# Kernel tuning notes

Measured on AMD Instinct MI355X. Metric: run time of the kernel, lower is better.

Reference implementation:

```python
import jax, jax.numpy as jnp
import numpy as np

KS = 4          # kernel_size per pseudo-dim (open linear B-splines, degree 1)
GRID = 28       # level-0 grid side
BATCH = 256     # number of graphs
NUM_FIRST_FC = 49


def _grid(n, B):
    """Batched 8-neighborhood grid graph with 2D pseudo-coords in [0,1]."""
    rs, cs = np.meshgrid(np.arange(n), np.arange(n), indexing='ij')
    idx = rs * n + cs
    src_l, dst_l, ps_l = [], [], []
    for dr in (-1, 0, 1):
        for dc in (-1, 0, 1):
            if dr == 0 and dc == 0:
                continue
            r2, c2 = rs + dr, cs + dc
            ok = (r2 >= 0) & (r2 < n) & (c2 >= 0) & (c2 < n)
            src_l.append(idx[ok])
            dst_l.append((r2 * n + c2)[ok])
            m = int(ok.sum())
            ps_l.append(np.stack([np.full(m, (dr + 1) / 2.0),
                                  np.full(m, (dc + 1) / 2.0)], 1))
    src = np.concatenate(src_l)
    dst = np.concatenate(dst_l)
    pseudo = np.concatenate(ps_l).astype(np.float32)
    off = (np.arange(B) * n * n)[:, None]
    src_b = (src[None] + off).reshape(-1)
    dst_b = (dst[None] + off).reshape(-1)
    return (np.stack([src_b, dst_b]).astype(np.int32),
            np.tile(pseudo, (B, 1)))


def _cluster(n, B):
    """Factor-4 (2x2 block) graclus-style cluster assignment, batched."""
    rs, cs = np.meshgrid(np.arange(n), np.arange(n), indexing='ij')
    c = ((rs // 2) * (n // 2) + (cs // 2)).reshape(-1)
    off = (np.arange(B) * (n // 2) ** 2)[:, None]
    return (c[None] + off).reshape(-1).astype(np.int32)


def setup_inputs() -> dict:
    key = jax.random.key(0)
    ks = jax.random.split(key, 16)
    e0, p0 = _grid(GRID, BATCH)          # 28x28 level
    e1, p1 = _grid(GRID // 2, BATCH)     # 14x14 level
    c0 = _cluster(GRID, BATCH)           # 784 -> 196 per graph
    c1 = _cluster(GRID // 2, BATCH)      # 196 -> 49 per graph
    N0 = BATCH * GRID * GRID
    s = 0.1
    inp = {
        'x': jax.random.normal(ks[0], (N0, 1), jnp.float32),
        'edge_index0': jnp.asarray(e0), 'pseudo0': jnp.asarray(p0),
        'edge_index1': jnp.asarray(e1), 'pseudo1': jnp.asarray(p1),
        'cluster0': jnp.asarray(c0), 'cluster1': jnp.asarray(c1),
        'W1': s * jax.random.normal(ks[1], (16, 1, 32), jnp.float32),
        'root1': s * jax.random.normal(ks[2], (1, 32), jnp.float32),
        'b1': jnp.zeros((32,), jnp.float32),
        'W2': s * jax.random.normal(ks[3], (16, 32, 32), jnp.float32),
        'root2': s * jax.random.normal(ks[4], (32, 32), jnp.float32),
        'b2': jnp.zeros((32,), jnp.float32),
        'W3': s * jax.random.normal(ks[5], (16, 32, 64), jnp.float32),
        'root3': s * jax.random.normal(ks[6], (32, 64), jnp.float32),
        'b3': jnp.zeros((64,), jnp.float32),
        'W4': s * jax.random.normal(ks[7], (16, 64, 64), jnp.float32),
        'root4': s * jax.random.normal(ks[8], (64, 64), jnp.float32),
        'b4': jnp.zeros((64,), jnp.float32),
        'fc1_W': s * jax.random.normal(ks[9], (NUM_FIRST_FC * 64, 512), jnp.float32),
        'fc1_b': jnp.zeros((512,), jnp.float32),
        'fc2_W': s * jax.random.normal(ks[10], (512, 10), jnp.float32),
        'fc2_b': jnp.zeros((10,), jnp.float32),
    }
    return inp


def spline_conv(x, src, dst, pseudo, W, root, bias):
    """SplineGCN layer: degree-1 open B-spline weighting over 2D pseudo-coords,
    mean aggregation over incoming edges, plus root weight and bias."""
    n = x.shape[0]
    pos = pseudo * (KS - 1)                       # [E,2] in [0, KS-1]
    i0f = jnp.clip(jnp.floor(pos), 0, KS - 2)
    frac = pos - i0f                              # [E,2]
    i0 = i0f.astype(jnp.int32)
    XW = jnp.einsum('ni,kio->kno', x, W)          # [K, N, out]: per-kernel transform
    msg = jnp.zeros((src.shape[0], W.shape[2]), x.dtype)
    for a in (0, 1):
        wa = frac[:, 0] if a else 1.0 - frac[:, 0]
        for b in (0, 1):
            wb = frac[:, 1] if b else 1.0 - frac[:, 1]
            k = (i0[:, 0] + a) * KS + (i0[:, 1] + b)     # flat kernel index [E]
            msg = msg + (wa * wb)[:, None] * XW[k, src]  # gather per-edge
    agg = jax.ops.segment_sum(msg, dst, num_segments=n)
    deg = jax.ops.segment_sum(jnp.ones_like(dst, dtype=x.dtype), dst,
                              num_segments=n)
    return agg / jnp.maximum(deg, 1.0)[:, None] + x @ root + bias


def pool4(x, cluster):
    # GraclusMaxPool(2): two halving levels == factor-4 cluster max-pool
    return jax.ops.segment_max(x, cluster, num_segments=x.shape[0] // 4)


def reference(x, edge_index0, pseudo0, edge_index1, pseudo1, cluster0, cluster1,
              W1, root1, b1, W2, root2, b2, W3, root3, b3, W4, root4, b4,
              fc1_W, fc1_b, fc2_W, fc2_b):
    s0, d0 = edge_index0[0], edge_index0[1]
    s1, d1 = edge_index1[0], edge_index1[1]
    h = jax.nn.elu(spline_conv(x, s0, d0, pseudo0, W1, root1, b1))
    h = jax.nn.elu(spline_conv(h, s0, d0, pseudo0, W2, root2, b2))
    h = pool4(h, cluster0)
    h = jax.nn.elu(spline_conv(h, s1, d1, pseudo1, W3, root3, b3))
    h = jax.nn.elu(spline_conv(h, s1, d1, pseudo1, W4, root4, b4))
    h = pool4(h, cluster1)
    h = h.reshape(-1, NUM_FIRST_FC * 64)           # [B, 49*64]
    h = jax.nn.elu(h @ fc1_W + fc1_b)
    # dropout is identity in eval / deterministic reference
    logits = h @ fc2_W + fc2_b
    return jax.nn.log_softmax(logits, axis=-1)
```

## Files before the change

kernel.cpp:

```cpp
#include <hip/hip_runtime.h>

typedef unsigned short u16;
typedef short bf16x8 __attribute__((ext_vector_type(8)));
typedef float f32x4 __attribute__((ext_vector_type(4)));

__device__ __constant__ const int DRS[8] = {-1,-1,-1, 0, 0, 1, 1, 1};
__device__ __constant__ const int DCS[8] = {-1, 0, 1,-1, 1,-1, 0, 1};

__device__ inline float bf2f(u16 u) { return __uint_as_float(((unsigned)u) << 16); }
__device__ inline u16 f2bf(float f) {
  unsigned u = __float_as_uint(f);
  return (u16)((u + 0x7fffu + ((u >> 16) & 1u)) >> 16);
}
__device__ inline float eluf(float v) { return v > 0.f ? v : (__expf(v) - 1.f); }
__device__ inline unsigned pk2(float a, float b) {
  return (unsigned)f2bf(a) | ((unsigned)f2bf(b) << 16);
}

__device__ inline float weff_val(const float* __restrict__ W, int d, int off, int stride) {
  int dd = d >= 4 ? d + 1 : d;
  int dr = dd / 3 - 1, dc = dd - (dd / 3) * 3 - 1;
  int kr0, kr1, nr; float wr0, wr1;
  if (dr < 0)       { kr0 = 0; wr0 = 1.f; kr1 = 0; wr1 = 0.f; nr = 1; }
  else if (dr == 0) { kr0 = 1; wr0 = .5f; kr1 = 2; wr1 = .5f; nr = 2; }
  else              { kr0 = 3; wr0 = 1.f; kr1 = 0; wr1 = 0.f; nr = 1; }
  int kc0, kc1, nc; float wc0, wc1;
  if (dc < 0)       { kc0 = 0; wc0 = 1.f; kc1 = 0; wc1 = 0.f; nc = 1; }
  else if (dc == 0) { kc0 = 1; wc0 = .5f; kc1 = 2; wc1 = .5f; nc = 2; }
  else              { kc0 = 3; wc0 = 1.f; kc1 = 0; wc1 = 0.f; nc = 1; }
  float acc = wr0 * wc0 * W[(kr0 * 4 + kc0) * stride + off];
  if (nc == 2) acc += wr0 * wc1 * W[(kr0 * 4 + kc1) * stride + off];
  if (nr == 2) {
    acc += wr1 * wc0 * W[(kr1 * 4 + kc0) * stride + off];
    if (nc == 2) acc += wr1 * wc1 * W[(kr1 * 4 + kc1) * stride + off];
  }
  return acc;
}

__device__ inline int kperm32(int p) { return (p >> 1) + ((p & 1) << 4); }

__global__ __launch_bounds__(256) void pack_all(
    const float* __restrict__ W1,
    const float* __restrict__ W2, const float* __restrict__ rt2,
    const float* __restrict__ W3, const float* __restrict__ rt3,
    const float* __restrict__ W4, const float* __restrict__ rt4,
    const float* __restrict__ fcW,
    float* __restrict__ wf1, u16* __restrict__ wp2,
    u16* __restrict__ wp3, u16* __restrict__ wp4, u16* __restrict__ wfc) {
  __shared__ u16 T[32 * 514];
  int blk = blockIdx.x, t = threadIdx.x;
  if (blk < 98) {
    int q = blk;
#pragma unroll
    for (int i = 0; i < 16; ++i) {
      int idx = i * 1024 + t * 4;
      int k = idx >> 9, n = idx & 511;
      float4 v = *reinterpret_cast<const float4*>(fcW + (size_t)(q * 32 + k) * 512 + n);
      T[k * 514 + n]     = f2bf(v.x);
      T[k * 514 + n + 1] = f2bf(v.y);
      T[k * 514 + n + 2] = f2bf(v.z);
      T[k * 514 + n + 3] = f2bf(v.w);
    }
    __syncthreads();
#pragma unroll
    for (int w = 0; w < 8; ++w) {
      int g = w * 256 + t;
      int nt = g >> 6, l = g & 63;
      union { int4 q4; u16 s[8]; } R;
#pragma unroll
      for (int j = 0; j < 8; ++j)
        R.s[j] = T[((l >> 4) * 8 + j) * 514 + nt * 16 + (l & 15)];
      *reinterpret_cast<int4*>(wfc + ((size_t)(q * 32 + nt) * 64 + l) * 8) = R.q4;
    }
    return;
  }
  int idx = (blk - 98) * 256 + t;
  if (idx < 256) {
    int d = idx >> 5, o = idx & 31;
    wf1[idx] = weff_val(W1, d, o, 32);
    return;
  }
  if (idx < 9472) {
    int local = idx - 256;
    int j = local & 7, l = (local >> 3) & 63, chunk = local >> 9;
    int ct = chunk & 1, tap = chunk >> 1;
    int k = (l >> 4) * 8 + j, n = ct * 16 + (l & 15);
    float v = tap < 8 ? weff_val(W2, tap, k * 32 + n, 1024) : rt2[k * 32 + n];
    wp2[local] = f2bf(v);
    return;
  }
  if (idx < 27904) {
    int local = idx - 9472;
    int j = local & 7, l = (local >> 3) & 63, chunk = local >> 9;
    int ct = chunk & 3, tap = chunk >> 2;
    int k = kperm32((l >> 4) * 8 + j), n = ct * 16 + (l & 15);
    float v = tap < 8 ? weff_val(W3, tap, k * 64 + n, 2048) : rt3[k * 64 + n];
    wp3[local] = f2bf(v);
    return;
  }
  if (idx < 64768) {
    int local = idx - 27904;
    int j = local & 7, l = (local >> 3) & 63, chunk = local >> 9;
    int q = chunk & 1, tmp = chunk >> 1;
    int ct = tmp & 3, tap = tmp >> 2;
    int k = q * 32 + kperm32((l >> 4) * 8 + j), n = ct * 16 + (l & 15);
    float v = tap < 8 ? weff_val(W4, tap, k * 64 + n, 4096) : rt4[k * 64 + n];
    wp4[local] = f2bf(v);
  }
}

__global__ __launch_bounds__(1024, 4) void conv_mega(
    const float* __restrict__ x,
    const float* __restrict__ wf1, const float* __restrict__ rt1, const float* __restrict__ b1,
    const u16* __restrict__ wp2, const float* __restrict__ b2,
    const u16* __restrict__ wp3, const float* __restrict__ b3,
    const u16* __restrict__ wp4, const float* __restrict__ b4,
    u16* __restrict__ A6) {
  extern __shared__ char smem[];
  int4* H1 = (int4*)smem;
  int4* H3 = (int4*)smem;
  u16*  H5 = (u16*)(smem + 17408);
  int4* H4 = (int4*)(smem + 42496);
  unsigned* H4u = (unsigned*)(smem + 42496);
  float* XT = (float*)(smem + 61568);
  int4*     H2 = (int4*)(smem + 75520);
  unsigned* H2u = (unsigned*)(smem + 75520);

  int img = blockIdx.x, tid = threadIdx.x;
  int lane = tid & 63, wid = tid >> 6;
  int kcb = lane >> 4, n0 = lane & 15;
  int4 z4 = make_int4(0, 0, 0, 0);
  f32x4 zz = {0.f, 0.f, 0.f, 0.f};

  for (int i = tid; i < 3848; i += 1024) H1[i] = z4;
  if (tid < 960) {
    int r = tid >> 5, c = tid & 31;
    bool in = (r >= 1) && (r <= 28) && (c >= 1) && (c <= 28);
    XT[tid] = in ? x[(size_t)img * 784 + (r - 1) * 28 + (c - 1)] : 0.f;
  }
  __syncthreads();

  if (tid < 784) {
    int px = tid;
    int r = px / 28, c = px - 28 * (px / 28);
    float acc[32];
#pragma unroll
    for (int o = 0; o < 32; ++o) acc[o] = 0.f;
#pragma unroll
    for (int d = 0; d < 8; ++d) {
      float xv = XT[(r + 1 - DRS[d]) * 32 + (c + 1 - DCS[d])];
#pragma unroll
      for (int o = 0; o < 32; ++o) acc[o] = fmaf(xv, wf1[d * 32 + o], acc[o]);
    }
    float inv = 1.f / (float)((3 - (r == 0) - (r == 27)) * (3 - (c == 0) - (c == 27)) - 1);
    float xc = XT[(r + 1) * 32 + c + 1];
    unsigned pk[16];
#pragma unroll
    for (int h = 0; h < 16; ++h)
      pk[h] = pk2(eluf(acc[2 * h] * inv + xc * rt1[2 * h] + b1[2 * h]),
                  eluf(acc[2 * h + 1] * inv + xc * rt1[2 * h + 1] + b1[2 * h + 1]));
#pragma unroll
    for (int kc = 0; kc < 4; ++kc)
      H1[kc * 962 + (r + 1) * 32 + (c + 1)] =
          make_int4(pk[4 * kc], pk[4 * kc + 1], pk[4 * kc + 2], pk[4 * kc + 3]);
  }
  __syncthreads();

  {
    bf16x8 w2[9][2];
#pragma unroll
    for (int tap = 0; tap < 9; ++tap)
#pragma unroll
      for (int ct = 0; ct < 2; ++ct)
        w2[tap][ct] = *(const bf16x8*)(wp2 + (tap * 2 + ct) * 512 + lane * 8);
    for (int t = wid; t < 49; t += 16) {
      int pxm = t * 16 + n0;
      int r = pxm / 28, c = pxm - 28 * (pxm / 28);
      f32x4 an[2] = {zz, zz}, ar[2] = {zz, zz};
#pragma unroll
      for (int d = 0; d < 8; ++d) {
        bf16x8 a = *(const bf16x8*)&H1[kcb * 962 + (r + 1 - DRS[d]) * 32 + (c + 1 - DCS[d])];
        an[0] = __builtin_amdgcn_mfma_f32_16x16x32_bf16(a, w2[d][0], an[0], 0, 0, 0);
        an[1] = __builtin_amdgcn_mfma_f32_16x16x32_bf16(a, w2[d][1], an[1], 0, 0, 0);
      }
      {
        bf16x8 a = *(const bf16x8*)&H1[kcb * 962 + (r + 1) * 32 + (c + 1)];
        ar[0] = __builtin_amdgcn_mfma_f32_16x16x32_bf16(a, w2[8][0], ar[0], 0, 0, 0);
        ar[1] = __builtin_amdgcn_mfma_f32_16x16x32_bf16(a, w2[8][1], ar[1], 0, 0, 0);
      }
#pragma unroll
      for (int j = 0; j < 4; ++j) {
        int pm = t * 16 + (lane >> 4) * 4 + j;
        int rm = pm / 28, cm = pm - 28 * (pm / 28);
        float inv = 1.f / (float)((3 - (rm == 0) - (rm == 27)) * (3 - (cm == 0) - (cm == 27)) - 1);
        H2u[pm * 16 + n0] = pk2(eluf(an[0][j] * inv + ar[0][j] + b2[n0]),
                                eluf(an[1][j] * inv + ar[1][j] + b2[16 + n0]));
      }
    }
  }
  __syncthreads();

  for (int i = tid; i < 1032; i += 1024) {
    int kc = i & 3, rem = i >> 2;
    int4 v = z4;
    if (rem < 256) {
      int pr = rem >> 4, pc = rem & 15;
      if (pr >= 1 && pr <= 14 && pc >= 1 && pc <= 14) {
        int px0 = (2 * (pr - 1)) * 28 + 2 * (pc - 1);
        union { int4 q; u16 s[8]; } A, B, C, D, R;
        A.q = H2[px0 * 4 + kc]; B.q = H2[(px0 + 1) * 4 + kc];
        C.q = H2[(px0 + 28) * 4 + kc]; D.q = H2[(px0 + 29) * 4 + kc];
#pragma unroll
        for (int e = 0; e < 8; ++e)
          R.s[e] = f2bf(fmaxf(fmaxf(bf2f(A.s[e]), bf2f(B.s[e])),
                              fmaxf(bf2f(C.s[e]), bf2f(D.s[e]))));
        v = R.q;
      }
    }
    H3[kc * 258 + rem] = v;
  }
  for (int i = tid; i < 2064; i += 1024) H4[i] = z4;
  __syncthreads();

  {
    int ct0 = wid & 1, t0 = wid >> 1;
    bf16x8 w3[9][2];
#pragma unroll
    for (int tap = 0; tap < 9; ++tap)
#pragma unroll
      for (int cc = 0; cc < 2; ++cc)
        w3[tap][cc] = *(const bf16x8*)(wp3 + (tap * 4 + ct0 * 2 + cc) * 512 + lane * 8);
    for (int t = t0; t < 13; t += 8) {
      int pxm = t * 16 + n0; if (pxm > 195) pxm = 195;
      int r = pxm / 14, c = pxm - 14 * (pxm / 14);
      f32x4 an[2] = {zz, zz}, ar[2] = {zz, zz};
#pragma unroll
      for (int d = 0; d < 8; ++d) {
        bf16x8 a = *(const bf16x8*)&H3[kcb * 258 + (r + 1 - DRS[d]) * 16 + (c + 1 - DCS[d])];
        an[0] = __builtin_amdgcn_mfma_f32_16x16x32_bf16(a, w3[d][0], an[0], 0, 0, 0);
        an[1] = __builtin_amdgcn_mfma_f32_16x16x32_bf16(a, w3[d][1], an[1], 0, 0, 0);
      }
      {
        bf16x8 a = *(const bf16x8*)&H3[kcb * 258 + (r + 1) * 16 + (c + 1)];
        ar[0] = __builtin_amdgcn_mfma_f32_16x16x32_bf16(a, w3[8][0], ar[0], 0, 0, 0);
        ar[1] = __builtin_amdgcn_mfma_f32_16x16x32_bf16(a, w3[8][1], ar[1], 0, 0, 0);
      }
#pragma unroll
      for (int j = 0; j < 4; ++j) {
        int pm = t * 16 + (lane >> 4) * 4 + j;
        if (pm < 196) {
          int rm = pm / 14, cm = pm - 14 * (pm / 14);
          float inv = 1.f / (float)((3 - (rm == 0) - (rm == 13)) * (3 - (cm == 0) - (cm == 13)) - 1);
          unsigned v = pk2(eluf(an[0][j] * inv + ar[0][j] + b3[ct0 * 32 + n0]),
                           eluf(an[1][j] * inv + ar[1][j] + b3[ct0 * 32 + 16 + n0]));
          H4u[((ct0 * 4 + (n0 >> 2)) * 258 + (rm + 1) * 16 + (cm + 1)) * 4 + (n0 & 3)] = v;
        }
      }
    }
  }
  __syncthreads();

  {
    int ctg = wid & 3, t0 = wid >> 2;
    bf16x8 w4[9][2];
#pragma unroll
    for (int tap = 0; tap < 9; ++tap)
#pragma unroll
      for (int kq = 0; kq < 2; ++kq)
        w4[tap][kq] = *(const bf16x8*)(wp4 + ((tap * 4 + ctg) * 2 + kq) * 512 + lane * 8);
    for (int t = t0; t < 13; t += 4) {
      int pxm = t * 16 + n0; if (pxm > 195) pxm = 195;
      int r = pxm / 14, c = pxm - 14 * (pxm / 14);
      f32x4 an = zz, ar = zz;
#pragma unroll
      for (int d = 0; d < 8; ++d) {
        int rr = r + 1 - DRS[d], c2 = c + 1 - DCS[d];
#pragma unroll
        for (int kq = 0; kq < 2; ++kq) {
          bf16x8 a = *(const bf16x8*)&H4[(kq * 4 + kcb) * 258 + rr * 16 + c2];
          an = __builtin_amdgcn_mfma_f32_16x16x32_bf16(a, w4[d][kq], an, 0, 0, 0);
        }
      }
#pragma unroll
      for (int kq = 0; kq < 2; ++kq) {
        bf16x8 a = *(const bf16x8*)&H4[(kq * 4 + kcb) * 258 + (r + 1) * 16 + (c + 1)];
        ar = __builtin_amdgcn_mfma_f32_16x16x32_bf16(a, w4[8][kq], ar, 0, 0, 0);
      }
#pragma unroll
      for (int j = 0; j < 4; ++j) {
        int pm = t * 16 + (lane >> 4) * 4 + j;
        if (pm < 196) {
          int rm = pm / 14, cm = pm - 14 * (pm / 14);
          float inv = 1.f / (float)((3 - (rm == 0) - (rm == 13)) * (3 - (cm == 0) - (cm == 13)) - 1);
          int n = ctg * 16 + n0;
          H5[pm * 64 + n] = f2bf(eluf(an[j] * inv + ar[j] + b4[n]));
        }
      }
    }
  }
  __syncthreads();

  if (tid < 392) {
    int kc = tid & 7, q = tid >> 3;
    int r2 = q / 7, c2 = q - 7 * (q / 7);
    int px0 = (2 * r2) * 14 + 2 * c2;
    union { int4 q4; u16 s[8]; } A, B, C, D, R;
    A.q4 = *(const int4*)&H5[px0 * 64 + kc * 8];
    B.q4 = *(const int4*)&H5[(px0 + 1) * 64 + kc * 8];
    C.q4 = *(const int4*)&H5[(px0 + 14) * 64 + kc * 8];
    D.q4 = *(const int4*)&H5[(px0 + 15) * 64 + kc * 8];
#pragma unroll
    for (int e = 0; e < 8; ++e)
      R.s[e] = f2bf(fmaxf(fmaxf(bf2f(A.s[e]), bf2f(B.s[e])),
                          fmaxf(bf2f(C.s[e]), bf2f(D.s[e]))));
    *(int4*)(A6 + ((size_t)img * 49 + q) * 64 + kc * 8) = R.q4;
  }
}

__global__ __launch_bounds__(256) void fc1_mfma(
    const u16* __restrict__ A6, const u16* __restrict__ wfc,
    float* __restrict__ part) {
  int blk = blockIdx.x;
  int ks = blk >> 5;
  int rem = blk & 31;
  int mt = rem & 3, nt4 = rem >> 2;
  int lane = threadIdx.x & 63, w = threadIdx.x >> 6;
  int NT = nt4 * 4 + w;
  f32x4 acc[4];
#pragma unroll
  for (int m4 = 0; m4 < 4; ++m4) acc[m4] = {0.f, 0.f, 0.f, 0.f};
  int rbase = mt * 64 + (lane & 15);
  int kb = ks * 224 + (lane >> 4) * 8;
#pragma unroll
  for (int qq = 0; qq < 7; ++qq) {
    bf16x8 bfr = *(const bf16x8*)(wfc + ((size_t)((ks * 7 + qq) * 32 + NT) * 64 + lane) * 8);
#pragma unroll
    for (int m4 = 0; m4 < 4; ++m4) {
      bf16x8 a = *(const bf16x8*)(A6 + (size_t)(rbase + m4 * 16) * 3136 + kb + qq * 32);
      acc[m4] = __builtin_amdgcn_mfma_f32_16x16x32_bf16(a, bfr, acc[m4], 0, 0, 0);
    }
  }
#pragma unroll
  for (int m4 = 0; m4 < 4; ++m4)
#pragma unroll
    for (int j = 0; j < 4; ++j) {
      int row = mt * 64 + m4 * 16 + (lane >> 4) * 4 + j;
      int col = NT * 16 + (lane & 15);
      part[((size_t)ks * 256 + row) * 512 + col] = acc[m4][j];
    }
}

__global__ __launch_bounds__(64) void fc2_kernel(
    const float* __restrict__ part, const float* __restrict__ fc1b,
    const float* __restrict__ W, const float* __restrict__ bias,
    float* __restrict__ out) {
  int bb = blockIdx.x;
  int t = threadIdx.x;
  float acc[10];
#pragma unroll
  for (int o = 0; o < 10; ++o) acc[o] = 0.f;
  for (int k = t; k < 512; k += 64) {
    float s = fc1b[k];
#pragma unroll
    for (int ks = 0; ks < 14; ++ks) s += part[(size_t)ks * 131072 + bb * 512 + k];
    float xv = eluf(s);
#pragma unroll
    for (int o = 0; o < 10; ++o) acc[o] = fmaf(xv, W[k * 10 + o], acc[o]);
  }
#pragma unroll
  for (int o = 0; o < 10; ++o) {
    float v = acc[o];
#pragma unroll
    for (int s = 32; s >= 1; s >>= 1) v += __shfl_xor(v, s);
    acc[o] = v + bias[o];
  }
  float m = acc[0];
#pragma unroll
  for (int o = 1; o < 10; ++o) m = fmaxf(m, acc[o]);
  float sum = 0.f;
#pragma unroll
  for (int o = 0; o < 10; ++o) sum += __expf(acc[o] - m);
  float lse = m + __logf(sum);
  if (t < 10) out[bb * 10 + t] = acc[t] - lse;
}

extern "C" void kernel_launch(void* const* d_in, const int* in_sizes, int n_in,
                              void* d_out, int out_size, void* d_ws, size_t ws_size,
                              hipStream_t stream) {
  const float* x    = (const float*)d_in[0];
  const float* W1   = (const float*)d_in[7];
  const float* r1   = (const float*)d_in[8];
  const float* b1   = (const float*)d_in[9];
  const float* W2   = (const float*)d_in[10];
  const float* r2   = (const float*)d_in[11];
  const float* b2   = (const float*)d_in[12];
  const float* W3   = (const float*)d_in[13];
  const float* r3   = (const float*)d_in[14];
  const float* b3   = (const float*)d_in[15];
  const float* W4   = (const float*)d_in[16];
  const float* r4   = (const float*)d_in[17];
  const float* b4   = (const float*)d_in[18];
  const float* fc1W = (const float*)d_in[19];
  const float* fc1b = (const float*)d_in[20];
  const float* fc2W = (const float*)d_in[21];
  const float* fc2b = (const float*)d_in[22];

  char* wsb = (char*)d_ws;
  float* wf1  = (float*)(wsb + 0);
  u16*   wp2  = (u16*)(wsb + 1024);
  u16*   wp3  = (u16*)(wsb + 19456);
  u16*   wp4  = (u16*)(wsb + 56320);
  u16*   wfc  = (u16*)(wsb + 130048);
  u16*   A6   = (u16*)(wsb + 3341312);
  float* part = (float*)(wsb + 4946944);

  pack_all<<<351, 256, 0, stream>>>(W1, W2, r2, W3, r3, W4, r4, fc1W,
                                    wf1, wp2, wp3, wp4, wfc);

  (void)hipFuncSetAttribute((const void*)conv_mega,
                            hipFuncAttributeMaxDynamicSharedMemorySize, 125696);
  conv_mega<<<256, 1024, 125696, stream>>>(x, wf1, r1, b1, wp2, b2, wp3, b3,
                                           wp4, b4, A6);

  fc1_mfma<<<448, 256, 0, stream>>>(A6, wfc, part);
  fc2_kernel<<<256, 64, 0, stream>>>(part, fc1b, fc2W, fc2b, (float*)d_out);
}
```

Before: 53.53 us.

## Prefetch conv weights across barriers, remap conv4 work, drop fc1 split-K

Conv2 and conv3 weight fragments are now loaded into registers before the preceding barrier, so global load latency overlaps the prior stage. Conv4 switches to the same 2-column-tile x 8-row-group wave mapping as conv3, loading weights per K-half inside the loop. fc1 now runs the full K reduction in one block per 16x32 output tile, fusing bias and ELU and writing bf16 activations. This removes the 14-way fp32 partial buffer and the reduction in fc2. The cost is longer serial K loops with less parallelism in fc1 and higher register pressure in the conv kernel.

```diff
diff --git a/kernel.cpp b/kernel.cpp
--- a/kernel.cpp
+++ b/kernel.cpp
@@ -129,6 +129,7 @@
   int img = blockIdx.x, tid = threadIdx.x;
   int lane = tid & 63, wid = tid >> 6;
   int kcb = lane >> 4, n0 = lane & 15;
+  int ct0 = wid & 1, t0 = wid >> 1;
   int4 z4 = make_int4(0, 0, 0, 0);
   f32x4 zz = {0.f, 0.f, 0.f, 0.f};
 
@@ -140,6 +141,13 @@
   }
   __syncthreads();
 
+  bf16x8 w2[9][2];
+#pragma unroll
+  for (int tap = 0; tap < 9; ++tap)
+#pragma unroll
+    for (int ct = 0; ct < 2; ++ct)
+      w2[tap][ct] = *(const bf16x8*)(wp2 + (tap * 2 + ct) * 512 + lane * 8);
+
   if (tid < 784) {
     int px = tid;
     int r = px / 28, c = px - 28 * (px / 28);
@@ -166,38 +174,37 @@
   }
   __syncthreads();
 
-  {
-    bf16x8 w2[9][2];
-#pragma unroll
-    for (int tap = 0; tap < 9; ++tap)
-#pragma unroll
-      for (int ct = 0; ct < 2; ++ct)
-        w2[tap][ct] = *(const bf16x8*)(wp2 + (tap * 2 + ct) * 512 + lane * 8);
-    for (int t = wid; t < 49; t += 16) {
-      int pxm = t * 16 + n0;
-      int r = pxm / 28, c = pxm - 28 * (pxm / 28);
-      f32x4 an[2] = {zz, zz}, ar[2] = {zz, zz};
-#pragma unroll
-      for (int d = 0; d < 8; ++d) {
-        bf16x8 a = *(const bf16x8*)&H1[kcb * 962 + (r + 1 - DRS[d]) * 32 + (c + 1 - DCS[d])];
-        an[0] = __builtin_amdgcn_mfma_f32_16x16x32_bf16(a, w2[d][0], an[0], 0, 0, 0);
-        an[1] = __builtin_amdgcn_mfma_f32_16x16x32_bf16(a, w2[d][1], an[1], 0, 0, 0);
-      }
-      {
-        bf16x8 a = *(const bf16x8*)&H1[kcb * 962 + (r + 1) * 32 + (c + 1)];
-        ar[0] = __builtin_amdgcn_mfma_f32_16x16x32_bf16(a, w2[8][0], ar[0], 0, 0, 0);
-        ar[1] = __builtin_amdgcn_mfma_f32_16x16x32_bf16(a, w2[8][1], ar[1], 0, 0, 0);
-      }
-#pragma unroll
-      for (int j = 0; j < 4; ++j) {
-        int pm = t * 16 + (lane >> 4) * 4 + j;
-        int rm = pm / 28, cm = pm - 28 * (pm / 28);
-        float inv = 1.f / (float)((3 - (rm == 0) - (rm == 27)) * (3 - (cm == 0) - (cm == 27)) - 1);
-        H2u[pm * 16 + n0] = pk2(eluf(an[0][j] * inv + ar[0][j] + b2[n0]),
-                                eluf(an[1][j] * inv + ar[1][j] + b2[16 + n0]));
-      }
-    }
-  }
+  for (int t = wid; t < 49; t += 16) {
+    int pxm = t * 16 + n0;
+    int r = pxm / 28, c = pxm - 28 * (pxm / 28);
+    f32x4 an[2] = {zz, zz}, ar[2] = {zz, zz};
+#pragma unroll
+    for (int d = 0; d < 8; ++d) {
+      bf16x8 a = *(const bf16x8*)&H1[kcb * 962 + (r + 1 - DRS[d]) * 32 + (c + 1 - DCS[d])];
+      an[0] = __builtin_amdgcn_mfma_f32_16x16x32_bf16(a, w2[d][0], an[0], 0, 0, 0);
+      an[1] = __builtin_amdgcn_mfma_f32_16x16x32_bf16(a, w2[d][1], an[1], 0, 0, 0);
+    }
+    {
+      bf16x8 a = *(const bf16x8*)&H1[kcb * 962 + (r + 1) * 32 + (c + 1)];
+      ar[0] = __builtin_amdgcn_mfma_f32_16x16x32_bf16(a, w2[8][0], ar[0], 0, 0, 0);
+      ar[1] = __builtin_amdgcn_mfma_f32_16x16x32_bf16(a, w2[8][1], ar[1], 0, 0, 0);
+    }
+#pragma unroll
+    for (int j = 0; j < 4; ++j) {
+      int pm = t * 16 + (lane >> 4) * 4 + j;
+      int rm = pm / 28, cm = pm - 28 * (pm / 28);
+      float inv = 1.f / (float)((3 - (rm == 0) - (rm == 27)) * (3 - (cm == 0) - (cm == 27)) - 1);
+      H2u[pm * 16 + n0] = pk2(eluf(an[0][j] * inv + ar[0][j] + b2[n0]),
+                              eluf(an[1][j] * inv + ar[1][j] + b2[16 + n0]));
+    }
+  }
+
+  bf16x8 w3[9][2];
+#pragma unroll
+  for (int tap = 0; tap < 9; ++tap)
+#pragma unroll
+    for (int cc = 0; cc < 2; ++cc)
+      w3[tap][cc] = *(const bf16x8*)(wp3 + (tap * 4 + ct0 * 2 + cc) * 512 + lane * 8);
   __syncthreads();
 
   for (int i = tid; i < 1032; i += 1024) {
@@ -222,79 +229,68 @@
   for (int i = tid; i < 2064; i += 1024) H4[i] = z4;
   __syncthreads();
 
-  {
-    int ct0 = wid & 1, t0 = wid >> 1;
-    bf16x8 w3[9][2];
-#pragma unroll
-    for (int tap = 0; tap < 9; ++tap)
-#pragma unroll
-      for (int cc = 0; cc < 2; ++cc)
-        w3[tap][cc] = *(const bf16x8*)(wp3 + (tap * 4 + ct0 * 2 + cc) * 512 + lane * 8);
-    for (int t = t0; t < 13; t += 8) {
-      int pxm = t * 16 + n0; if (pxm > 195) pxm = 195;
-      int r = pxm / 14, c = pxm - 14 * (pxm / 14);
-      f32x4 an[2] = {zz, zz}, ar[2] = {zz, zz};
+  for (int t = t0; t < 13; t += 8) {
+    int pxm = t * 16 + n0; if (pxm > 195) pxm = 195;
+    int r = pxm / 14, c = pxm - 14 * (pxm / 14);
+    f32x4 an[2] = {zz, zz}, ar[2] = {zz, zz};
+#pragma unroll
+    for (int d = 0; d < 8; ++d) {
+      bf16x8 a = *(const bf16x8*)&H3[kcb * 258 + (r + 1 - DRS[d]) * 16 + (c + 1 - DCS[d])];
+      an[0] = __builtin_amdgcn_mfma_f32_16x16x32_bf16(a, w3[d][0], an[0], 0, 0, 0);
+      an[1] = __builtin_amdgcn_mfma_f32_16x16x32_bf16(a, w3[d][1], an[1], 0, 0, 0);
+    }
+    {
+      bf16x8 a = *(const bf16x8*)&H3[kcb * 258 + (r + 1) * 16 + (c + 1)];
+      ar[0] = __builtin_amdgcn_mfma_f32_16x16x32_bf16(a, w3[8][0], ar[0], 0, 0, 0);
+      ar[1] = __builtin_amdgcn_mfma_f32_16x16x32_bf16(a, w3[8][1], ar[1], 0, 0, 0);
+    }
+#pragma unroll
+    for (int j = 0; j < 4; ++j) {
+      int pm = t * 16 + (lane >> 4) * 4 + j;
+      if (pm < 196) {
+        int rm = pm / 14, cm = pm - 14 * (pm / 14);
+        float inv = 1.f / (float)((3 - (rm == 0) - (rm == 13)) * (3 - (cm == 0) - (cm == 13)) - 1);
+        unsigned v = pk2(eluf(an[0][j] * inv + ar[0][j] + b3[ct0 * 32 + n0]),
+                         eluf(an[1][j] * inv + ar[1][j] + b3[ct0 * 32 + 16 + n0]));
+        H4u[((ct0 * 4 + (n0 >> 2)) * 258 + (rm + 1) * 16 + (cm + 1)) * 4 + (n0 & 3)] = v;
+      }
+    }
+  }
+  __syncthreads();
+
+  for (int t = t0; t < 13; t += 8) {
+    int pxm = t * 16 + n0; if (pxm > 195) pxm = 195;
+    int r = pxm / 14, c = pxm - 14 * (pxm / 14);
+    f32x4 an[2] = {zz, zz}, ar[2] = {zz, zz};
+#pragma unroll
+    for (int kq = 0; kq < 2; ++kq) {
+      bf16x8 w4[9][2];
+#pragma unroll
+      for (int tap = 0; tap < 9; ++tap)
+#pragma unroll
+        for (int cc = 0; cc < 2; ++cc)
+          w4[tap][cc] = *(const bf16x8*)(wp4 + ((tap * 4 + ct0 * 2 + cc) * 2 + kq) * 512 + lane * 8);
 #pragma unroll
       for (int d = 0; d < 8; ++d) {
-        bf16x8 a = *(const bf16x8*)&H3[kcb * 258 + (r + 1 - DRS[d]) * 16 + (c + 1 - DCS[d])];
-        an[0] = __builtin_amdgcn_mfma_f32_16x16x32_bf16(a, w3[d][0], an[0], 0, 0, 0);
-        an[1] = __builtin_amdgcn_mfma_f32_16x16x32_bf16(a, w3[d][1], an[1], 0, 0, 0);
+        bf16x8 a = *(const bf16x8*)&H4[(kq * 4 + kcb) * 258 + (r + 1 - DRS[d]) * 16 + (c + 1 - DCS[d])];
+        an[0] = __builtin_amdgcn_mfma_f32_16x16x32_bf16(a, w4[d][0], an[0], 0, 0, 0);
+        an[1] = __builtin_amdgcn_mfma_f32_16x16x32_bf16(a, w4[d][1], an[1], 0, 0, 0);
       }
       {
-        bf16x8 a = *(const bf16x8*)&H3[kcb * 258 + (r + 1) * 16 + (c + 1)];
-        ar[0] = __builtin_amdgcn_mfma_f32_16x16x32_bf16(a, w3[8][0], ar[0], 0, 0, 0);
-        ar[1] = __builtin_amdgcn_mfma_f32_16x16x32_bf16(a, w3[8][1], ar[1], 0, 0, 0);
+        bf16x8 a = *(const bf16x8*)&H4[(kq * 4 + kcb) * 258 + (r + 1) * 16 + (c + 1)];
+        ar[0] = __builtin_amdgcn_mfma_f32_16x16x32_bf16(a, w4[8][0], ar[0], 0, 0, 0);
+        ar[1] = __builtin_amdgcn_mfma_f32_16x16x32_bf16(a, w4[8][1], ar[1], 0, 0, 0);
       }
-#pragma unroll
-      for (int j = 0; j < 4; ++j) {
-        int pm = t * 16 + (lane >> 4) * 4 + j;
-        if (pm < 196) {
-          int rm = pm / 14, cm = pm - 14 * (pm / 14);
-          float inv = 1.f / (float)((3 - (rm == 0) - (rm == 13)) * (3 - (cm == 0) - (cm == 13)) - 1);
-          unsigned v = pk2(eluf(an[0][j] * inv + ar[0][j] + b3[ct0 * 32 + n0]),
-                           eluf(an[1][j] * inv + ar[1][j] + b3[ct0 * 32 + 16 + n0]));
-          H4u[((ct0 * 4 + (n0 >> 2)) * 258 + (rm + 1) * 16 + (cm + 1)) * 4 + (n0 & 3)] = v;
-        }
-      }
-    }
-  }
-  __syncthreads();
-
-  {
-    int ctg = wid & 3, t0 = wid >> 2;
-    bf16x8 w4[9][2];
-#pragma unroll
-    for (int tap = 0; tap < 9; ++tap)
-#pragma unroll
-      for (int kq = 0; kq < 2; ++kq)
-        w4[tap][kq] = *(const bf16x8*)(wp4 + ((tap * 4 + ctg) * 2 + kq) * 512 + lane * 8);
-    for (int t = t0; t < 13; t += 4) {
-      int pxm = t * 16 + n0; if (pxm > 195) pxm = 195;
-      int r = pxm / 14, c = pxm - 14 * (pxm / 14);
-      f32x4 an = zz, ar = zz;
-#pragma unroll
-      for (int d = 0; d < 8; ++d) {
-        int rr = r + 1 - DRS[d], c2 = c + 1 - DCS[d];
-#pragma unroll
-        for (int kq = 0; kq < 2; ++kq) {
-          bf16x8 a = *(const bf16x8*)&H4[(kq * 4 + kcb) * 258 + rr * 16 + c2];
-          an = __builtin_amdgcn_mfma_f32_16x16x32_bf16(a, w4[d][kq], an, 0, 0, 0);
-        }
-      }
-#pragma unroll
-      for (int kq = 0; kq < 2; ++kq) {
-        bf16x8 a = *(const bf16x8*)&H4[(kq * 4 + kcb) * 258 + (r + 1) * 16 + (c + 1)];
-        ar = __builtin_amdgcn_mfma_f32_16x16x32_bf16(a, w4[8][kq], ar, 0, 0, 0);
-      }
-#pragma unroll
-      for (int j = 0; j < 4; ++j) {
-        int pm = t * 16 + (lane >> 4) * 4 + j;
-        if (pm < 196) {
-          int rm = pm / 14, cm = pm - 14 * (pm / 14);
-          float inv = 1.f / (float)((3 - (rm == 0) - (rm == 13)) * (3 - (cm == 0) - (cm == 13)) - 1);
-          int n = ctg * 16 + n0;
-          H5[pm * 64 + n] = f2bf(eluf(an[j] * inv + ar[j] + b4[n]));
-        }
+    }
+#pragma unroll
+    for (int j = 0; j < 4; ++j) {
+      int pm = t * 16 + (lane >> 4) * 4 + j;
+      if (pm < 196) {
+        int rm = pm / 14, cm = pm - 14 * (pm / 14);
+        float inv = 1.f / (float)((3 - (rm == 0) - (rm == 13)) * (3 - (cm == 0) - (cm == 13)) - 1);
+        int na = ct0 * 32 + n0, nb = ct0 * 32 + 16 + n0;
+        H5[pm * 64 + na] = f2bf(eluf(an[0][j] * inv + ar[0][j] + b4[na]));
+        H5[pm * 64 + nb] = f2bf(eluf(an[1][j] * inv + ar[1][j] + b4[nb]));
       }
     }
   }
@@ -317,53 +313,47 @@
   }
 }
 
-__global__ __launch_bounds__(256) void fc1_mfma(
+__global__ __launch_bounds__(128) void fc1_mfma(
     const u16* __restrict__ A6, const u16* __restrict__ wfc,
-    float* __restrict__ part) {
+    const float* __restrict__ fc1b, u16* __restrict__ h) {
   int blk = blockIdx.x;
-  int ks = blk >> 5;
-  int rem = blk & 31;
-  int mt = rem & 3, nt4 = rem >> 2;
+  int mt = blk & 15, bn = blk >> 4;
   int lane = threadIdx.x & 63, w = threadIdx.x >> 6;
-  int NT = nt4 * 4 + w;
-  f32x4 acc[4];
-#pragma unroll
-  for (int m4 = 0; m4 < 4; ++m4) acc[m4] = {0.f, 0.f, 0.f, 0.f};
-  int rbase = mt * 64 + (lane & 15);
-  int kb = ks * 224 + (lane >> 4) * 8;
-#pragma unroll
-  for (int qq = 0; qq < 7; ++qq) {
-    bf16x8 bfr = *(const bf16x8*)(wfc + ((size_t)((ks * 7 + qq) * 32 + NT) * 64 + lane) * 8);
-#pragma unroll
-    for (int m4 = 0; m4 < 4; ++m4) {
-      bf16x8 a = *(const bf16x8*)(A6 + (size_t)(rbase + m4 * 16) * 3136 + kb + qq * 32);
-      acc[m4] = __builtin_amdgcn_mfma_f32_16x16x32_bf16(a, bfr, acc[m4], 0, 0, 0);
-    }
-  }
-#pragma unroll
-  for (int m4 = 0; m4 < 4; ++m4)
-#pragma unroll
-    for (int j = 0; j < 4; ++j) {
-      int row = mt * 64 + m4 * 16 + (lane >> 4) * 4 + j;
-      int col = NT * 16 + (lane & 15);
-      part[((size_t)ks * 256 + row) * 512 + col] = acc[m4][j];
-    }
+  int NT = bn * 2 + w;
+  f32x4 acc0 = {0.f, 0.f, 0.f, 0.f}, acc1 = {0.f, 0.f, 0.f, 0.f};
+  const u16* Ab = A6 + (size_t)(mt * 16 + (lane & 15)) * 3136 + (lane >> 4) * 8;
+  const u16* Bb = wfc + (size_t)NT * 512 + (size_t)lane * 8;
+#pragma unroll 7
+  for (int qq = 0; qq < 98; qq += 2) {
+    bf16x8 a0 = *(const bf16x8*)(Ab + qq * 32);
+    bf16x8 b0 = *(const bf16x8*)(Bb + (size_t)qq * 16384);
+    acc0 = __builtin_amdgcn_mfma_f32_16x16x32_bf16(a0, b0, acc0, 0, 0, 0);
+    bf16x8 a1 = *(const bf16x8*)(Ab + qq * 32 + 32);
+    bf16x8 b1 = *(const bf16x8*)(Bb + (size_t)qq * 16384 + 16384);
+    acc1 = __builtin_amdgcn_mfma_f32_16x16x32_bf16(a1, b1, acc1, 0, 0, 0);
+  }
+#pragma unroll
+  for (int j = 0; j < 4; ++j) {
+    int row = mt * 16 + (lane >> 4) * 4 + j;
+    int col = NT * 16 + (lane & 15);
+    float v = acc0[j] + acc1[j] + fc1b[col];
+    h[(size_t)row * 512 + col] = f2bf(eluf(v));
+  }
 }
 
 __global__ __launch_bounds__(64) void fc2_kernel(
-    const float* __restrict__ part, const float* __restrict__ fc1b,
-    const float* __restrict__ W, const float* __restrict__ bias,
-    float* __restrict__ out) {
+    const u16* __restrict__ h, const float* __restrict__ W,
+    const float* __restrict__ bias, float* __restrict__ out) {
   int bb = blockIdx.x;
   int t = threadIdx.x;
   float acc[10];
 #pragma unroll
   for (int o = 0; o < 10; ++o) acc[o] = 0.f;
-  for (int k = t; k < 512; k += 64) {
-    float s = fc1b[k];
-#pragma unroll
-    for (int ks = 0; ks < 14; ++ks) s += part[(size_t)ks * 131072 + bb * 512 + k];
-    float xv = eluf(s);
+  bf16x8 hv = *(const bf16x8*)(h + (size_t)bb * 512 + t * 8);
+#pragma unroll
+  for (int kk = 0; kk < 8; ++kk) {
+    float xv = bf2f((u16)hv[kk]);
+    int k = t * 8 + kk;
 #pragma unroll
     for (int o = 0; o < 10; ++o) acc[o] = fmaf(xv, W[k * 10 + o], acc[o]);
   }
@@ -412,7 +402,7 @@
   u16*   wp4  = (u16*)(wsb + 56320);
   u16*   wfc  = (u16*)(wsb + 130048);
   u16*   A6   = (u16*)(wsb + 3341312);
-  float* part = (float*)(wsb + 4946944);
+  u16*   hbuf = (u16*)(wsb + 4946944);
 
   pack_all<<<351, 256, 0, stream>>>(W1, W2, r2, W3, r3, W4, r4, fc1W,
                                     wf1, wp2, wp3, wp4, wfc);
@@ -422,6 +412,6 @@
   conv_mega<<<256, 1024, 125696, stream>>>(x, wf1, r1, b1, wp2, b2, wp3, b3,
                                            wp4, b4, A6);
 
-  fc1_mfma<<<448, 256, 0, stream>>>(A6, wfc, part);
-  fc2_kernel<<<256, 64, 0, stream>>>(part, fc1b, fc2W, fc2b, (float*)d_out);
-}
+  fc1_mfma<<<256, 128, 0, stream>>>(A6, wfc, fc1b, hbuf);
+  fc2_kernel<<<256, 64, 0, stream>>>(hbuf, fc2W, fc2b, (float*)d_out);
+}
```

Result: slower. 80.42 us (+50.2%).
